# Kernel tuning notes

Hardware: AMD Instinct MI355X
Metric: run time of the kernel (lower is better)

The kernel has to match this reference:

```python
import jax, jax.numpy as jnp
import numpy as np

N, E, D_IN, H, D_HEAD = 50000, 800000, 128, 8, 16
SCALE = float(np.sqrt(D_HEAD))


def setup_inputs() -> dict:
    key = jax.random.key(0)
    ks = jax.random.split(key, 9)
    h = jax.random.normal(ks[0], (N, D_IN), dtype=jnp.float32)
    # Q/K/V projection params (torch Linear: y = x @ W.T + b; store as [D_IN, H*D_HEAD])
    s = 1.0 / np.sqrt(D_IN)
    Wq = jax.random.uniform(ks[1], (D_IN, H * D_HEAD), minval=-s, maxval=s, dtype=jnp.float32)
    Wk = jax.random.uniform(ks[2], (D_IN, H * D_HEAD), minval=-s, maxval=s, dtype=jnp.float32)
    Wv = jax.random.uniform(ks[3], (D_IN, H * D_HEAD), minval=-s, maxval=s, dtype=jnp.float32)
    bq = jax.random.uniform(ks[4], (H * D_HEAD,), minval=-s, maxval=s, dtype=jnp.float32)
    bk = jax.random.uniform(ks[5], (H * D_HEAD,), minval=-s, maxval=s, dtype=jnp.float32)
    bv = jax.random.uniform(ks[6], (H * D_HEAD,), minval=-s, maxval=s, dtype=jnp.float32)
    src = jax.random.randint(ks[7], (E,), 0, N, dtype=jnp.int32)
    dst = jax.random.randint(ks[8], (E,), 0, N, dtype=jnp.int32)
    return {"h": h, "Wq": Wq, "bq": bq, "Wk": Wk, "bk": bk, "Wv": Wv, "bv": bv,
            "src": src, "dst": dst}


def reference(h, Wq, bq, Wk, bk, Wv, bv, src, dst):
    n = h.shape[0]
    Q = (h @ Wq + bq).reshape(n, H, D_HEAD)
    K = (h @ Wk + bk).reshape(n, H, D_HEAD)
    V = (h @ Wv + bv).reshape(n, H, D_HEAD)
    # per-edge dot-product score: (K_src * Q_dst).sum(-1), clamped exp
    score = jnp.sum(K[src] * Q[dst], axis=-1, keepdims=True)  # [E, H, 1]
    score = jnp.exp(jnp.clip(score / SCALE, -5.0, 5.0))
    # segment-sum weighted aggregation to destination nodes
    wV = jax.ops.segment_sum(V[src] * score, dst, num_segments=n)   # [N, H, D_HEAD]
    z = jax.ops.segment_sum(score, dst, num_segments=n)              # [N, H, 1]
    return wV / (z + 1e-6)
```

## Files before the change

kernel.cpp:

```cpp
#include <hip/hip_runtime.h>
#include <hip/hip_bf16.h>

#define N_NODES 50000
#define N_EDGES 800000
#define DIN     128
#define HD      128
#define NHEAD   8
#define DHEAD   16

#define M_PAD        53248
#define HIST_BLOCKS  3125
#define CVTW_BLOCKS  192
#define PROJ_BLOCKS  391
#define SCAT_BLOCKS  3125
#define AGG_BLOCKS   12500

typedef __attribute__((ext_vector_type(8))) short short8;
typedef __attribute__((ext_vector_type(4))) float float4v;

static __device__ __forceinline__ unsigned short f2bf_bits(float f) {
    __hip_bfloat16 b = __float2bfloat16(f);
    return *reinterpret_cast<unsigned short*>(&b);
}
static __device__ __forceinline__ float bfb(short b) {
    return __uint_as_float(((unsigned int)(unsigned short)b) << 16);
}
static __device__ __forceinline__ short8 cvt8(const float* p) {
    const float4 f0 = *(const float4*)p;
    const float4 f1 = *(const float4*)(p + 4);
    short8 r;
    r[0] = (short)f2bf_bits(f0.x); r[1] = (short)f2bf_bits(f0.y);
    r[2] = (short)f2bf_bits(f0.z); r[3] = (short)f2bf_bits(f0.w);
    r[4] = (short)f2bf_bits(f1.x); r[5] = (short)f2bf_bits(f1.y);
    r[6] = (short)f2bf_bits(f1.z); r[7] = (short)f2bf_bits(f1.w);
    return r;
}

__global__ __launch_bounds__(256) void hist_cvtw_kernel(
    const int* __restrict__ dst,
    const float* __restrict__ Wq, const float* __restrict__ Wk,
    const float* __restrict__ Wv,
    int* __restrict__ counts, int* __restrict__ rank,
    unsigned short* __restrict__ Wt)
{
    const int bid = blockIdx.x;
    if (bid < HIST_BLOCKS) {
        const int e = bid * 256 + threadIdx.x;
        if (e < N_EDGES) rank[e] = atomicAdd(&counts[dst[e]], 1);
    } else {
        const int i   = (bid - HIST_BLOCKS) * 256 + threadIdx.x;
        const int n   = i & 127;
        const int k   = (i >> 7) & 127;
        const int mat = i >> 14;
        const float* W = (mat == 0) ? Wq : (mat == 1) ? Wk : Wv;
        Wt[mat * (DIN * HD) + n * DIN + k] = f2bf_bits(W[k * HD + n]);
    }
}

__global__ __launch_bounds__(1024) void scan_kernel(
    const int* __restrict__ counts, int* __restrict__ cursor)
{
    __shared__ int s[1024];
    const int tid  = threadIdx.x;
    const int base = tid * 52;

    int4 c[13];
    const int4* c4 = (const int4*)(counts + base);
    int sum = 0;
    #pragma unroll
    for (int g = 0; g < 13; ++g) {
        c[g] = c4[g];
        sum += c[g].x + c[g].y + c[g].z + c[g].w;
    }

    s[tid] = sum;
    __syncthreads();
    for (int off = 1; off < 1024; off <<= 1) {
        int x = (tid >= off) ? s[tid - off] : 0;
        __syncthreads();
        s[tid] += x;
        __syncthreads();
    }
    int excl = s[tid] - sum;

    int4* o4 = (int4*)(cursor + base);
    #pragma unroll
    for (int g = 0; g < 13; ++g) {
        int4 o;
        o.x = excl; excl += c[g].x;
        o.y = excl; excl += c[g].y;
        o.z = excl; excl += c[g].z;
        o.w = excl; excl += c[g].w;
        o4[g] = o;
    }
}

__global__ __launch_bounds__(256) void proj_scatter_kernel(
    const float* __restrict__ h,
    const unsigned short* __restrict__ Wt,
    const float* __restrict__ bq, const float* __restrict__ bk,
    const float* __restrict__ bv,
    const int* __restrict__ src, const int* __restrict__ dst,
    const int* __restrict__ cursor, const int* __restrict__ rank,
    __hip_bfloat16* __restrict__ Qb, __hip_bfloat16* __restrict__ KV,
    int* __restrict__ sorted_src)
{
    const int bid = blockIdx.x;
    if (bid >= PROJ_BLOCKS) {
        const int e = (bid - PROJ_BLOCKS) * 256 + threadIdx.x;
        if (e < N_EDGES) {
            const int pos = cursor[dst[e]] + rank[e];
            sorted_src[pos] = src[e];
        }
        return;
    }

    const int wave = threadIdx.x >> 6;
    const int lane = threadIdx.x & 63;
    const int quad = lane >> 4;
    const int l16  = lane & 15;
    const int rowBase = bid * 128 + wave * 32;

    int r0 = rowBase + l16;       if (r0 >= N_NODES) r0 = N_NODES - 1;
    int r1 = rowBase + 16 + l16;  if (r1 >= N_NODES) r1 = N_NODES - 1;

    short8 afr[2][4];
    #pragma unroll
    for (int kc = 0; kc < 4; ++kc) {
        const int ko = kc * 32 + quad * 8;
        afr[0][kc] = cvt8(h + (size_t)r0 * DIN + ko);
        afr[1][kc] = cvt8(h + (size_t)r1 * DIN + ko);
    }

    #pragma unroll
    for (int mat = 0; mat < 3; ++mat) {
        const unsigned short* wb = Wt + mat * (DIN * HD);
        const float* bias = (mat == 0) ? bq : (mat == 1) ? bk : bv;

        float4v acc[2][8];
        #pragma unroll
        for (int rt = 0; rt < 2; ++rt)
            #pragma unroll
            for (int ct = 0; ct < 8; ++ct)
                acc[rt][ct] = (float4v){0.f, 0.f, 0.f, 0.f};

        #pragma unroll
        for (int kc = 0; kc < 4; ++kc) {
            const int ko = kc * 32 + quad * 8;
            #pragma unroll
            for (int ct = 0; ct < 8; ++ct) {
                const short8 b = *(const short8*)(wb + (ct * 16 + l16) * DIN + ko);
                acc[0][ct] = __builtin_amdgcn_mfma_f32_16x16x32_bf16(afr[0][kc], b, acc[0][ct], 0, 0, 0);
                acc[1][ct] = __builtin_amdgcn_mfma_f32_16x16x32_bf16(afr[1][kc], b, acc[1][ct], 0, 0, 0);
            }
        }

        #pragma unroll
        for (int ct = 0; ct < 8; ++ct) {
            const int col = ct * 16 + l16;
            const float bcol = bias[col];
            #pragma unroll
            for (int rt = 0; rt < 2; ++rt) {
                #pragma unroll
                for (int r = 0; r < 4; ++r) {
                    const int row = rowBase + rt * 16 + quad * 4 + r;
                    if (row < N_NODES) {
                        const float v = acc[rt][ct][r] + bcol;
                        if (mat == 0)
                            Qb[(size_t)row * HD + col] = __float2bfloat16(v);
                        else
                            KV[(size_t)row * 256 + (mat == 2 ? 128 : 0) + col] =
                                __float2bfloat16(v);
                    }
                }
            }
        }
    }
}

__global__ __launch_bounds__(256) void aggregate_kernel(
    const __hip_bfloat16* __restrict__ Qb, const __hip_bfloat16* __restrict__ KV,
    const int* __restrict__ cursor, const int* __restrict__ counts,
    const int* __restrict__ sorted_src, float* __restrict__ out)
{
    const int w    = threadIdx.x >> 6;
    const int node = blockIdx.x * 4 + w;
    const int lane = threadIdx.x & 63;
    const int quad = lane >> 4;
    const int l16  = lane & 15;
    const int hB   = lane >> 3;

    const int beg = cursor[node];
    const int end = beg + counts[node];

    __shared__ float sc_s[4][2][16][9];
    __shared__ int   s_s[4][2][16];

    const short* qrow = (const short*)Qb + (size_t)node * HD;
    const short8 zero8 = {0, 0, 0, 0, 0, 0, 0, 0};
    short8 bfr[4];
    #pragma unroll
    for (int kc = 0; kc < 4; ++kc) {
        const int head = kc * 2 + (quad >> 1);
        const short8 qv = *(const short8*)(qrow + quad * 8 + kc * 32);
        bfr[kc] = (l16 == head) ? qv : zero8;
    }

    const short* kvb = (const short*)KV;
    float acc0 = 0.f, acc1 = 0.f, zacc = 0.f;

    int buf = 0;
    for (int e0 = beg; e0 < end; e0 += 16, buf ^= 1) {
        const int nb = min(16, end - e0);

        const int eidx = e0 + l16;
        const int s = (eidx < end) ? sorted_src[eidx] : 0;
        if (quad == 0) s_s[w][buf][l16] = s;

        const short* kp = kvb + (size_t)s * 256 + quad * 8;
        float4v acc4 = {0.f, 0.f, 0.f, 0.f};
        #pragma unroll
        for (int kc = 0; kc < 4; ++kc) {
            const short8 a = *(const short8*)(kp + kc * 32);
            acc4 = __builtin_amdgcn_mfma_f32_16x16x32_bf16(a, bfr[kc], acc4, 0, 0, 0);
        }
        if (l16 < 8) {
            #pragma unroll
            for (int r = 0; r < 4; ++r) {
                const float d = acc4[r] * 0.25f;
                sc_s[w][buf][quad * 4 + r][l16] =
                    __expf(fminf(fmaxf(d, -5.f), 5.f));
            }
        }
        __threadfence_block();

        int j = 0;
        for (; j + 3 < nb; j += 4) {
            const int s0 = s_s[w][buf][j],     s1 = s_s[w][buf][j + 1];
            const int s2 = s_s[w][buf][j + 2], s3 = s_s[w][buf][j + 3];
            const float c0 = sc_s[w][buf][j][hB],     c1 = sc_s[w][buf][j + 1][hB];
            const float c2 = sc_s[w][buf][j + 2][hB], c3 = sc_s[w][buf][j + 3][hB];
            const unsigned int v0 = *(const unsigned int*)(kvb + (size_t)s0 * 256 + 128 + 2 * lane);
            const unsigned int v1 = *(const unsigned int*)(kvb + (size_t)s1 * 256 + 128 + 2 * lane);
            const unsigned int v2 = *(const unsigned int*)(kvb + (size_t)s2 * 256 + 128 + 2 * lane);
            const unsigned int v3 = *(const unsigned int*)(kvb + (size_t)s3 * 256 + 128 + 2 * lane);
            acc0 = fmaf(__uint_as_float(v0 << 16), c0, acc0);
            acc1 = fmaf(__uint_as_float(v0 & 0xffff0000u), c0, acc1);
            acc0 = fmaf(__uint_as_float(v1 << 16), c1, acc0);
            acc1 = fmaf(__uint_as_float(v1 & 0xffff0000u), c1, acc1);
            acc0 = fmaf(__uint_as_float(v2 << 16), c2, acc0);
            acc1 = fmaf(__uint_as_float(v2 & 0xffff0000u), c2, acc1);
            acc0 = fmaf(__uint_as_float(v3 << 16), c3, acc0);
            acc1 = fmaf(__uint_as_float(v3 & 0xffff0000u), c3, acc1);
            zacc += (c0 + c1) + (c2 + c3);
        }
        for (; j < nb; ++j) {
            const int s0 = s_s[w][buf][j];
            const float c0 = sc_s[w][buf][j][hB];
            const unsigned int v0 = *(const unsigned int*)(kvb + (size_t)s0 * 256 + 128 + 2 * lane);
            acc0 = fmaf(__uint_as_float(v0 << 16), c0, acc0);
            acc1 = fmaf(__uint_as_float(v0 & 0xffff0000u), c0, acc1);
            zacc += c0;
        }
    }

    const float inv = 1.f / (zacc + 1e-6f);
    float2 o;
    o.x = acc0 * inv;
    o.y = acc1 * inv;
    *(float2*)(out + (size_t)node * HD + 2 * lane) = o;
}

extern "C" void kernel_launch(void* const* d_in, const int* in_sizes, int n_in,
                              void* d_out, int out_size, void* d_ws, size_t ws_size,
                              hipStream_t stream)
{
    const float* h   = (const float*)d_in[0];
    const float* Wq  = (const float*)d_in[1];
    const float* bq  = (const float*)d_in[2];
    const float* Wk  = (const float*)d_in[3];
    const float* bk  = (const float*)d_in[4];
    const float* Wv  = (const float*)d_in[5];
    const float* bv  = (const float*)d_in[6];
    const int*   src = (const int*)d_in[7];
    const int*   dst = (const int*)d_in[8];
    float* out = (float*)d_out;

    __hip_bfloat16* Qb = (__hip_bfloat16*)d_ws;
    __hip_bfloat16* KV = Qb + (size_t)N_NODES * HD;
    unsigned short* Wt = (unsigned short*)(KV + (size_t)N_NODES * 256);
    int* counts     = (int*)(Wt + 3 * DIN * HD);
    int* cursor     = counts + M_PAD;
    int* sorted_src = cursor + M_PAD;
    int* rank       = sorted_src + N_EDGES;

    hipMemsetAsync(counts, 0, M_PAD * sizeof(int), stream);

    hist_cvtw_kernel<<<HIST_BLOCKS + CVTW_BLOCKS, 256, 0, stream>>>(
        dst, Wq, Wk, Wv, counts, rank, Wt);

    scan_kernel<<<1, 1024, 0, stream>>>(counts, cursor);

    proj_scatter_kernel<<<PROJ_BLOCKS + SCAT_BLOCKS, 256, 0, stream>>>(
        h, Wt, bq, bk, bv, src, dst, cursor, rank, Qb, KV, sorted_src);

    aggregate_kernel<<<AGG_BLOCKS, 256, 0, stream>>>(
        Qb, KV, cursor, counts, sorted_src, out);
}
```

Measured before the change: 247.6 us.

## Split QKV projection across blocks per matrix and stage weights in LDS

```diff
diff --git a/kernel.cpp b/kernel.cpp
--- a/kernel.cpp
+++ b/kernel.cpp
@@ -11,7 +11,7 @@
 #define M_PAD        53248
 #define HIST_BLOCKS  3125
 #define CVTW_BLOCKS  192
-#define PROJ_BLOCKS  391
+#define PROJ3_BLOCKS 1173
 #define SCAT_BLOCKS  3125
 #define AGG_BLOCKS   12500
 
@@ -106,20 +106,38 @@
     int* __restrict__ sorted_src)
 {
     const int bid = blockIdx.x;
-    if (bid >= PROJ_BLOCKS) {
-        const int e = (bid - PROJ_BLOCKS) * 256 + threadIdx.x;
+    if (bid >= PROJ3_BLOCKS) {
+        const int e = (bid - PROJ3_BLOCKS) * 256 + threadIdx.x;
         if (e < N_EDGES) {
             const int pos = cursor[dst[e]] + rank[e];
             sorted_src[pos] = src[e];
         }
         return;
     }
+
+    const int mat  = bid % 3;
+    const int tile = bid / 3;
+
+    __shared__ unsigned short wlds[DIN * HD];
+    {
+        const unsigned short* wg = Wt + mat * (DIN * HD);
+        #pragma unroll
+        for (int it = 0; it < 8; ++it) {
+            const int idx = it * 256 + threadIdx.x;
+            const int row = idx >> 4;
+            const int ch  = idx & 15;
+            const int cu  = ((ch >> 2) * 8 + (row >> 4)) * 64
+                          + (ch & 3) * 16 + (row & 15);
+            *(short8*)&wlds[cu * 8] = *(const short8*)(wg + idx * 8);
+        }
+    }
+    __syncthreads();
 
     const int wave = threadIdx.x >> 6;
     const int lane = threadIdx.x & 63;
     const int quad = lane >> 4;
     const int l16  = lane & 15;
-    const int rowBase = bid * 128 + wave * 32;
+    const int rowBase = tile * 128 + wave * 32;
 
     int r0 = rowBase + l16;       if (r0 >= N_NODES) r0 = N_NODES - 1;
     int r1 = rowBase + 16 + l16;  if (r1 >= N_NODES) r1 = N_NODES - 1;
@@ -132,46 +150,42 @@
         afr[1][kc] = cvt8(h + (size_t)r1 * DIN + ko);
     }
 
-    #pragma unroll
-    for (int mat = 0; mat < 3; ++mat) {
-        const unsigned short* wb = Wt + mat * (DIN * HD);
-        const float* bias = (mat == 0) ? bq : (mat == 1) ? bk : bv;
-
-        float4v acc[2][8];
-        #pragma unroll
-        for (int rt = 0; rt < 2; ++rt)
+    const float* bias = (mat == 0) ? bq : (mat == 1) ? bk : bv;
+
+    float4v acc[2][8];
+    #pragma unroll
+    for (int rt = 0; rt < 2; ++rt)
+        #pragma unroll
+        for (int ct = 0; ct < 8; ++ct)
+            acc[rt][ct] = (float4v){0.f, 0.f, 0.f, 0.f};
+
+    #pragma unroll
+    for (int kc = 0; kc < 4; ++kc) {
+        #pragma unroll
+        for (int ct = 0; ct < 8; ++ct) {
+            const int cu = (kc * 8 + ct) * 64 + lane;
+            const short8 b = *(const short8*)&wlds[cu * 8];
+            acc[0][ct] = __builtin_amdgcn_mfma_f32_16x16x32_bf16(afr[0][kc], b, acc[0][ct], 0, 0, 0);
+            acc[1][ct] = __builtin_amdgcn_mfma_f32_16x16x32_bf16(afr[1][kc], b, acc[1][ct], 0, 0, 0);
+        }
+    }
+
+    #pragma unroll
+    for (int ct = 0; ct < 8; ++ct) {
+        const int col = ct * 16 + l16;
+        const float bcol = bias[col];
+        #pragma unroll
+        for (int rt = 0; rt < 2; ++rt) {
             #pragma unroll
-            for (int ct = 0; ct < 8; ++ct)
-                acc[rt][ct] = (float4v){0.f, 0.f, 0.f, 0.f};
-
-        #pragma unroll
-        for (int kc = 0; kc < 4; ++kc) {
-            const int ko = kc * 32 + quad * 8;
-            #pragma unroll
-            for (int ct = 0; ct < 8; ++ct) {
-                const short8 b = *(const short8*)(wb + (ct * 16 + l16) * DIN + ko);
-                acc[0][ct] = __builtin_amdgcn_mfma_f32_16x16x32_bf16(afr[0][kc], b, acc[0][ct], 0, 0, 0);
-                acc[1][ct] = __builtin_amdgcn_mfma_f32_16x16x32_bf16(afr[1][kc], b, acc[1][ct], 0, 0, 0);
-            }
-        }
-
-        #pragma unroll
-        for (int ct = 0; ct < 8; ++ct) {
-            const int col = ct * 16 + l16;
-            const float bcol = bias[col];
-            #pragma unroll
-            for (int rt = 0; rt < 2; ++rt) {
-                #pragma unroll
-                for (int r = 0; r < 4; ++r) {
-                    const int row = rowBase + rt * 16 + quad * 4 + r;
-                    if (row < N_NODES) {
-                        const float v = acc[rt][ct][r] + bcol;
-                        if (mat == 0)
-                            Qb[(size_t)row * HD + col] = __float2bfloat16(v);
-                        else
-                            KV[(size_t)row * 256 + (mat == 2 ? 128 : 0) + col] =
-                                __float2bfloat16(v);
-                    }
+            for (int r = 0; r < 4; ++r) {
+                const int row = rowBase + rt * 16 + quad * 4 + r;
+                if (row < N_NODES) {
+                    const float v = acc[rt][ct][r] + bcol;
+                    if (mat == 0)
+                        Qb[(size_t)row * HD + col] = __float2bfloat16(v);
+                    else
+                        KV[(size_t)row * 256 + (mat == 2 ? 128 : 0) + col] =
+                            __float2bfloat16(v);
                 }
             }
         }
@@ -301,7 +315,7 @@
 
     scan_kernel<<<1, 1024, 0, stream>>>(counts, cursor);
 
-    proj_scatter_kernel<<<PROJ_BLOCKS + SCAT_BLOCKS, 256, 0, stream>>>(
+    proj_scatter_kernel<<<PROJ3_BLOCKS + SCAT_BLOCKS, 256, 0, stream>>>(
         h, Wt, bq, bk, bv, src, dst, cursor, rank, Qb, KV, sorted_src);
 
     aggregate_kernel<<<AGG_BLOCKS, 256, 0, stream>>>(
```

Measured after the change: 239.0 us. 1.04x faster.
